# Kernel optimization log

Hardware: AMD Instinct MI355X
Metric: run time of the kernel (lower is better)

## Reference

```python
import jax, jax.numpy as jnp
import numpy as np

N = 20000        # nodes
E = 640000       # edges
D = 128          # embed_dim
L = 3            # num_layers
NUM_PROTEINS_MASK = 21
BN_EPS = 1e-5


def _batchnorm(x, gamma, beta):
    # training-mode BatchNorm1d: biased batch statistics over axis 0
    mu = jnp.mean(x, axis=0)
    var = jnp.mean((x - mu) ** 2, axis=0)
    return (x - mu) * jax.lax.rsqrt(var + BN_EPS) * gamma + beta


def setup_inputs() -> dict:
    key = jax.random.key(0)
    ks = jax.random.split(key, 20)
    s = 0.05
    return {
        "x_tokens": jax.random.randint(ks[0], (N,), 0, NUM_PROTEINS_MASK),
        "edge_index": jax.random.randint(ks[1], (2, E), 0, N),
        "edge_attr": jax.random.normal(ks[2], (E, D), jnp.float32),
        "emb": jax.random.normal(ks[3], (NUM_PROTEINS_MASK, D), jnp.float32) * s,
        "ee_W": jax.random.normal(ks[4], (L, D, D), jnp.float32) * s,
        "ee_b": jnp.zeros((L, D), jnp.float32),
        "W1": jax.random.normal(ks[5], (L, D, 2 * D), jnp.float32) * s,
        "b1": jnp.zeros((L, 2 * D), jnp.float32),
        "bn1_g": jnp.ones((L, 2 * D), jnp.float32),
        "bn1_b": jnp.zeros((L, 2 * D), jnp.float32),
        "W2": jax.random.normal(ks[6], (L, 2 * D, D), jnp.float32) * s,
        "b2": jnp.zeros((L, D), jnp.float32),
        "eps_p": jnp.zeros((L,), jnp.float32),
        "bn_g": jnp.ones((L, D), jnp.float32),
        "bn_b": jnp.zeros((L, D), jnp.float32),
    }


def reference(x_tokens, edge_index, edge_attr, emb, ee_W, ee_b, W1, b1,
              bn1_g, bn1_b, W2, b2, eps_p, bn_g, bn_b):
    src = edge_index[0]  # x_j is gathered from edge_index[0] (PyG source_to_target)
    dst = edge_index[1]
    h = emb[x_tokens]  # [N, D]
    for l in range(L):
        # GINConv: edge encode, gather-message-scatter
        ea = edge_attr @ ee_W[l] + ee_b[l]                      # [E, D]
        msg = jax.nn.relu(h[src] + ea)                          # [E, D]
        agg = jax.ops.segment_sum(msg, dst, num_segments=N)     # [N, D]
        z = (1.0 + eps_p[l]) * h + agg
        # MLP: Linear -> BN -> ReLU -> Linear
        z = _batchnorm(z @ W1[l] + b1[l], bn1_g[l], bn1_b[l])
        z = jax.nn.relu(z)
        h = z @ W2[l] + b2[l]
        # outer BatchNorm; ReLU except last layer; dropout p=0 -> identity
        h = _batchnorm(h, bn_g[l], bn_b[l])
        if l < L - 1:
            h = jax.nn.relu(h)
    return h
```

## Files before the change

### kernel.cpp

```cpp
#include <hip/hip_runtime.h>
#include <stdint.h>

#define NN 20000
#define EE 640000
#define DDIM 128
#define D2 256
#define NLAY 3
#define BN_EPS 1e-5f

typedef short bf16x8 __attribute__((ext_vector_type(8)));
typedef float f32x4 __attribute__((ext_vector_type(4)));

__device__ __forceinline__ short f2bf(float f) {
    uint32_t u = __float_as_uint(f);
    u += 0x7fff + ((u >> 16) & 1);
    return (short)(u >> 16);
}
__device__ __forceinline__ float bf2f(uint32_t u16) {
    return __uint_as_float(u16 << 16);
}

__global__ __launch_bounds__(256) void k_embed_hist(const int* __restrict__ tok,
                                                    const float* __restrict__ emb,
                                                    float* __restrict__ h,
                                                    const int* __restrict__ ei,
                                                    int* __restrict__ counts) {
    int gid = blockIdx.x * 256 + threadIdx.x;
    int r = gid >> 5;
    int c4 = gid & 31;
    int t = tok[r];
    ((float4*)h)[gid] = ((const float4*)emb)[t * 32 + c4];
    atomicAdd(&counts[ei[EE + gid]], 1);
}

__global__ __launch_bounds__(1024) void k_scan(const int* __restrict__ counts, int* __restrict__ cursor) {
    __shared__ int buf[NN];
    __shared__ int part[1024];
    int t = threadIdx.x;
    for (int i = t; i < NN; i += 1024) buf[i] = counts[i];
    __syncthreads();
    int base = t * 20;
    int s = 0;
    #pragma unroll
    for (int i = 0; i < 20; i++) {
        int idx = base + i;
        if (idx < NN) s += buf[idx];
    }
    part[t] = s;
    __syncthreads();
    for (int off = 1; off < 1024; off <<= 1) {
        int v = (t >= off) ? part[t - off] : 0;
        __syncthreads();
        part[t] += v;
        __syncthreads();
    }
    int run = part[t] - s;
    #pragma unroll
    for (int i = 0; i < 20; i++) {
        int idx = base + i;
        if (idx < NN) { int c = buf[idx]; buf[idx] = run; run += c; }
    }
    __syncthreads();
    for (int i = t; i < NN; i += 1024) cursor[i] = buf[i];
}

__global__ __launch_bounds__(256) void k_scatter(const int* __restrict__ ei,
                                                 int* __restrict__ cursor,
                                                 int* __restrict__ perm,
                                                 int* __restrict__ rank) {
    int e = blockIdx.x * 256 + threadIdx.x;
    int d = ei[EE + e];
    int pos = atomicAdd(&cursor[d], 1);
    perm[pos] = e;
    rank[e] = pos;
}

__global__ __launch_bounds__(256) void k_permute2(const float* __restrict__ edge_attr,
                                                  const int* __restrict__ ei,
                                                  const int* __restrict__ rank,
                                                  short* __restrict__ ea_bf,
                                                  int* __restrict__ srcs,
                                                  int* __restrict__ dsts) {
    int gid = blockIdx.x * 256 + threadIdx.x;
    int e = gid >> 5, c4 = gid & 31;
    float4 v = ((const float4*)edge_attr)[gid];
    int pos = rank[e];
    short4 b;
    b.x = f2bf(v.x); b.y = f2bf(v.y); b.z = f2bf(v.z); b.w = f2bf(v.w);
    ((short4*)ea_bf)[(size_t)pos * 32 + c4] = b;
    if (c4 == 0) { srcs[pos] = ei[e]; dsts[pos] = ei[EE + e]; }
}

__global__ __launch_bounds__(256) void k_prepw_all(const float* __restrict__ eeW,
                                                   const float* __restrict__ W1,
                                                   const float* __restrict__ W2,
                                                   short* __restrict__ WtE,
                                                   short* __restrict__ W1t,
                                                   short* __restrict__ W2t) {
    int gid = blockIdx.x * 256 + threadIdx.x;
    const int T1 = NLAY * 128 * 128;
    const int T2 = NLAY * 128 * 256;
    const int T3 = NLAY * 256 * 128;
    if (gid < T1) {
        int l = gid / (128 * 128), rem = gid % (128 * 128);
        int k = rem >> 7, n = rem & 127;
        WtE[(l * 128 + n) * 128 + k] = f2bf(eeW[gid]);
    } else if (gid < T1 + T2) {
        int g = gid - T1;
        int l = g / (128 * 256), rem = g % (128 * 256);
        int k = rem >> 8, n = rem & 255;
        W1t[(l * 256 + n) * 128 + k] = f2bf(W1[g]);
    } else if (gid < T1 + T2 + T3) {
        int g = gid - T1 - T2;
        int l = g / (256 * 128), rem = g % (256 * 128);
        int k = rem >> 7, n = rem & 127;
        W2t[(l * 128 + n) * 256 + k] = f2bf(W2[g]);
    }
}

__global__ __launch_bounds__(256) void k_edge3(const short* __restrict__ ea_bf,
                                               const int* __restrict__ srcs,
                                               const int* __restrict__ dsts,
                                               const short* __restrict__ WtL,
                                               const float* __restrict__ ebL,
                                               const float* __restrict__ hbase,
                                               const float* __restrict__ st2,
                                               const float* __restrict__ g2,
                                               const float* __restrict__ b2v,
                                               int lazy,
                                               float* __restrict__ agg) {
    __shared__ __align__(16) short sW[128 * 136];
    __shared__ __align__(16) short sOutB[64 * 132];
    __shared__ int sSrc[64], sDst[64];
    int tid = threadIdx.x;

    const uint2* wg = (const uint2*)WtL;
    #pragma unroll
    for (int i = 0; i < 16; i++) {
        int idx = tid + i * 256;
        uint2 v = wg[idx];
        int n = idx >> 5, k4 = (idx & 31) << 2;
        *(uint2*)&sW[n * 136 + k4] = v;
    }
    int lane = tid & 63, wv = tid >> 6;
    int l15 = lane & 15, quad = lane >> 4;
    int r0 = wv * 16;

    float ebv[8];
    #pragma unroll
    for (int nt = 0; nt < 8; nt++) ebv[nt] = ebL[nt * 16 + l15];

    int pc2 = tid & 63;
    int pc = pc2 * 2;
    int prb = tid >> 6;
    float ls0 = 0.f, ls1 = 0.f, lt0 = 0.f, lt1 = 0.f;
    if (lazy) {
        float inv_n = 1.f / (float)NN;
        float mu0 = st2[pc] * inv_n,     mu1 = st2[pc + 1] * inv_n;
        float va0 = st2[128 + pc] * inv_n - mu0 * mu0;
        float va1 = st2[129 + pc] * inv_n - mu1 * mu1;
        ls0 = g2[pc] * rsqrtf(va0 + BN_EPS);     lt0 = b2v[pc] - mu0 * ls0;
        ls1 = g2[pc + 1] * rsqrtf(va1 + BN_EPS); lt1 = b2v[pc + 1] - mu1 * ls1;
    }

    #pragma unroll 1
    for (int sub = 0; sub < 4; sub++) {
        int tile = blockIdx.x * 4 + sub;
        if (tid < 64) {
            sSrc[tid] = srcs[tile * 64 + tid];
            sDst[tid] = dsts[tile * 64 + tid];
        }
        const short* abase = ea_bf + ((size_t)(tile * 64 + r0 + l15)) * 128 + quad * 8;
        bf16x8 a[4];
        #pragma unroll
        for (int kt = 0; kt < 4; kt++) a[kt] = *(const bf16x8*)(abase + kt * 32);
        if (sub == 0) __syncthreads();

        f32x4 acc[8];
        #pragma unroll
        for (int i = 0; i < 8; i++) acc[i] = (f32x4){0.f, 0.f, 0.f, 0.f};
        #pragma unroll
        for (int kt = 0; kt < 4; kt++) {
            #pragma unroll
            for (int nt = 0; nt < 8; nt++) {
                bf16x8 b = *(const bf16x8*)&sW[(nt * 16 + l15) * 136 + kt * 32 + quad * 8];
                acc[nt] = __builtin_amdgcn_mfma_f32_16x16x32_bf16(a[kt], b, acc[nt], 0, 0, 0);
            }
        }
        #pragma unroll
        for (int nt = 0; nt < 8; nt++) {
            #pragma unroll
            for (int reg = 0; reg < 4; reg++)
                sOutB[(r0 + quad * 4 + reg) * 132 + nt * 16 + l15] = f2bf(acc[nt][reg] + ebv[nt]);
        }
        __syncthreads();

        #pragma unroll
        for (int i = 0; i < 16; i++) {
            int r = prb + i * 4;
            float2 hv = *(const float2*)&hbase[(size_t)sSrc[r] * DDIM + pc];
            float h0, h1;
            if (lazy) {
                h0 = fmaxf(hv.x * ls0 + lt0, 0.f);
                h1 = fmaxf(hv.y * ls1 + lt1, 0.f);
            } else {
                h0 = hv.x; h1 = hv.y;
            }
            uint32_t pp = *(uint32_t*)&sOutB[r * 132 + pc];
            float m0 = fmaxf(bf2f(pp & 0xffffu) + h0, 0.f);
            float m1 = fmaxf(bf2f(pp >> 16) + h1, 0.f);
            uint32_t po = (uint32_t)(uint16_t)f2bf(m0) | ((uint32_t)(uint16_t)f2bf(m1) << 16);
            *(uint32_t*)&sOutB[r * 132 + pc] = po;
        }
        __syncthreads();
        int c = tid & 127;
        int rbeg = (tid >> 7) * 32;
        float s = 0.f;
        int cur = sDst[rbeg];
        for (int r = rbeg; r < rbeg + 32; r++) {
            int d = sDst[r];
            if (d != cur) { atomicAdd(&agg[(size_t)cur * DDIM + c], s); s = 0.f; cur = d; }
            uint32_t raw = *(const uint16_t*)&sOutB[r * 132 + c];
            s += bf2f(raw);
        }
        atomicAdd(&agg[(size_t)cur * DDIM + c], s);
        if (sub < 3) __syncthreads();
    }
}

__global__ __launch_bounds__(256) void k_edge_g(const float* __restrict__ edge_attr,
                                                const short* __restrict__ WtL,
                                                const float* __restrict__ ebL,
                                                const float* __restrict__ h,
                                                const int* __restrict__ ei,
                                                const int* __restrict__ perm,
                                                float* __restrict__ agg) {
    __shared__ __align__(16) short sW[128 * 136];
    __shared__ __align__(16) char sU[64 * 132 * 4];
    __shared__ int sSrc[64], sDst[64], sEdge[64];
    short* sA = (short*)sU;
    float* sOut = (float*)sU;
    int tid = threadIdx.x;
    int tile = blockIdx.x;
    if (tid < 64) {
        int e = perm[tile * 64 + tid];
        sEdge[tid] = e;
        sSrc[tid] = ei[e];
        sDst[tid] = ei[EE + e];
    }
    const uint2* wg = (const uint2*)WtL;
    #pragma unroll
    for (int i = 0; i < 16; i++) {
        int idx = tid + i * 256;
        uint2 v = wg[idx];
        int n = idx >> 5, k4 = (idx & 31) << 2;
        *(uint2*)&sW[n * 136 + k4] = v;
    }
    __syncthreads();
    #pragma unroll
    for (int i = 0; i < 8; i++) {
        int idx = tid + i * 256;
        int r = idx >> 5, c4 = idx & 31;
        float4 v = ((const float4*)edge_attr)[sEdge[r] * 32 + c4];
        short4 b;
        b.x = f2bf(v.x); b.y = f2bf(v.y); b.z = f2bf(v.z); b.w = f2bf(v.w);
        *(short4*)&sA[r * 136 + (c4 << 2)] = b;
    }
    __syncthreads();
    int lane = tid & 63, wv = tid >> 6;
    int l15 = lane & 15, quad = lane >> 4;
    int r0 = wv * 16;
    f32x4 acc[8];
    #pragma unroll
    for (int i = 0; i < 8; i++) acc[i] = (f32x4){0.f, 0.f, 0.f, 0.f};
    #pragma unroll
    for (int kt = 0; kt < 4; kt++) {
        bf16x8 a = *(const bf16x8*)&sA[(r0 + l15) * 136 + kt * 32 + quad * 8];
        #pragma unroll
        for (int nt = 0; nt < 8; nt++) {
            bf16x8 b = *(const bf16x8*)&sW[(nt * 16 + l15) * 136 + kt * 32 + quad * 8];
            acc[nt] = __builtin_amdgcn_mfma_f32_16x16x32_bf16(a, b, acc[nt], 0, 0, 0);
        }
    }
    __syncthreads();
    #pragma unroll
    for (int nt = 0; nt < 8; nt++)
        #pragma unroll
        for (int reg = 0; reg < 4; reg++)
            sOut[(r0 + quad * 4 + reg) * 132 + nt * 16 + l15] = acc[nt][reg];
    __syncthreads();
    #pragma unroll
    for (int i = 0; i < 32; i++) {
        int idx = tid + i * 256;
        int r = idx >> 7, c = idx & 127;
        float v = sOut[r * 132 + c] + ebL[c] + h[(size_t)sSrc[r] * DDIM + c];
        sOut[r * 132 + c] = fmaxf(v, 0.f);
    }
    __syncthreads();
    int c = tid & 127;
    int rbeg = (tid >> 7) * 32;
    float s = 0.f;
    int cur = sDst[rbeg];
    for (int r = rbeg; r < rbeg + 32; r++) {
        int d = sDst[r];
        if (d != cur) { atomicAdd(&agg[(size_t)cur * DDIM + c], s); s = 0.f; cur = d; }
        s += sOut[r * 132 + c];
    }
    atomicAdd(&agg[(size_t)cur * DDIM + c], s);
}

__global__ __launch_bounds__(256) void k_gemm1z(const float* __restrict__ hbase,
                                                const float* __restrict__ st2,
                                                const float* __restrict__ g2,
                                                const float* __restrict__ b2v,
                                                int lazy,
                                                const float* __restrict__ agg,
                                                const float* __restrict__ epsP, int l,
                                                const short* __restrict__ W1tL,
                                                float* __restrict__ zz,
                                                float* __restrict__ stats) {
    __shared__ __align__(16) short sB[128 * 136];
    __shared__ __align__(16) short sA[64 * 136];
    int tid = threadIdx.x;
    int tile = blockIdx.x;
    int half = blockIdx.y;
    float e1 = 1.f + epsP[l];
    const uint2* bg = (const uint2*)W1tL + (size_t)half * 128 * 32;
    #pragma unroll
    for (int i = 0; i < 16; i++) {
        int idx = tid + i * 256;
        uint2 v = bg[idx];
        int n = idx >> 5, k4 = (idx & 31) << 2;
        *(uint2*)&sB[n * 136 + k4] = v;
    }
    {
        int c4 = tid & 31;
        int c = c4 * 4;
        float scv[4] = {0.f, 0.f, 0.f, 0.f}, shv[4] = {0.f, 0.f, 0.f, 0.f};
        if (lazy) {
            float inv_n = 1.f / (float)NN;
            #pragma unroll
            for (int j = 0; j < 4; j++) {
                float mu = st2[c + j] * inv_n;
                float var = st2[128 + c + j] * inv_n - mu * mu;
                float sc = g2[c + j] * rsqrtf(var + BN_EPS);
                scv[j] = sc;
                shv[j] = b2v[c + j] - mu * sc;
            }
        }
        #pragma unroll
        for (int i = 0; i < 8; i++) {
            int idx = tid + i * 256;
            int r = idx >> 5;
            int gr = tile * 64 + r;
            short4 o = {0, 0, 0, 0};
            if (gr < NN) {
                float4 hv = ((const float4*)hbase)[gr * 32 + c4];
                if (lazy) {
                    hv.x = fmaxf(hv.x * scv[0] + shv[0], 0.f);
                    hv.y = fmaxf(hv.y * scv[1] + shv[1], 0.f);
                    hv.z = fmaxf(hv.z * scv[2] + shv[2], 0.f);
                    hv.w = fmaxf(hv.w * scv[3] + shv[3], 0.f);
                }
                float4 av = ((const float4*)agg)[gr * 32 + c4];
                o.x = f2bf(e1 * hv.x + av.x);
                o.y = f2bf(e1 * hv.y + av.y);
                o.z = f2bf(e1 * hv.z + av.z);
                o.w = f2bf(e1 * hv.w + av.w);
            }
            *(short4*)&sA[r * 136 + c] = o;
        }
    }
    __syncthreads();
    int lane = tid & 63, wv = tid >> 6;
    int l15 = lane & 15, quad = lane >> 4;
    int r0 = wv * 16;
    f32x4 acc[8];
    #pragma unroll
    for (int i = 0; i < 8; i++) acc[i] = (f32x4){0.f, 0.f, 0.f, 0.f};
    #pragma unroll
    for (int kt = 0; kt < 4; kt++) {
        bf16x8 a = *(const bf16x8*)&sA[(r0 + l15) * 136 + kt * 32 + quad * 8];
        #pragma unroll
        for (int nt = 0; nt < 8; nt++) {
            bf16x8 b = *(const bf16x8*)&sB[(nt * 16 + l15) * 136 + kt * 32 + quad * 8];
            acc[nt] = __builtin_amdgcn_mfma_f32_16x16x32_bf16(a, b, acc[nt], 0, 0, 0);
        }
    }
    int grb = tile * 64 + r0 + quad * 4;
    #pragma unroll
    for (int nt = 0; nt < 8; nt++) {
        int col = half * 128 + nt * 16 + l15;
        float s = 0.f, s2 = 0.f;
        #pragma unroll
        for (int reg = 0; reg < 4; reg++) {
            int gr = grb + reg;
            float v = acc[nt][reg];
            s += v; s2 += v * v;
            if (gr < NN) zz[(size_t)gr * D2 + col] = v;
        }
        s += __shfl_xor(s, 16);  s += __shfl_xor(s, 32);
        s2 += __shfl_xor(s2, 16); s2 += __shfl_xor(s2, 32);
        if (quad == 0) {
            atomicAdd(&stats[col], s);
            atomicAdd(&stats[D2 + col], s2);
        }
    }
}

__global__ __launch_bounds__(256) void k_gemm2s(const float* __restrict__ zz,
                                                const short* __restrict__ W2tL,
                                                const float* __restrict__ st1,
                                                const float* __restrict__ g1,
                                                const float* __restrict__ b1v,
                                                float* __restrict__ h_pre,
                                                float* __restrict__ stats) {
    __shared__ __align__(16) short sB[64 * 136];
    __shared__ __align__(16) short sA[64 * 136];
    __shared__ float sSc[256], sSh[256];
    int tid = threadIdx.x;
    int tile = blockIdx.x;
    int half = blockIdx.y;
    int lane = tid & 63, wv = tid >> 6;
    int l15 = lane & 15, quad = lane >> 4;
    int r0 = wv * 16;
    f32x4 acc[4];
    #pragma unroll
    for (int i = 0; i < 4; i++) acc[i] = (f32x4){0.f, 0.f, 0.f, 0.f};

    #pragma unroll 1
    for (int p = 0; p < 2; p++) {
        if (p == 0) {
            float inv_n = 1.f / (float)NN;
            float mu = st1[tid] * inv_n;
            float var = st1[256 + tid] * inv_n - mu * mu;
            float sc = g1[tid] * rsqrtf(var + BN_EPS);
            sSc[tid] = sc;
            sSh[tid] = b1v[tid] - mu * sc;
            const uint2* bg = (const uint2*)W2tL + (size_t)half * 64 * 64;
            #pragma unroll
            for (int i = 0; i < 8; i++) {
                int idx = tid + i * 256;
                int n = idx >> 5, k4q = idx & 31;
                uint2 v = bg[n * 64 + k4q];
                *(uint2*)&sB[n * 136 + k4q * 4] = v;
            }
            __syncthreads();
        } else {
            __syncthreads();
            const uint2* bg = (const uint2*)W2tL + (size_t)half * 64 * 64 + 32;
            #pragma unroll
            for (int i = 0; i < 8; i++) {
                int idx = tid + i * 256;
                int n = idx >> 5, k4q = idx & 31;
                uint2 v = bg[n * 64 + k4q];
                *(uint2*)&sB[n * 136 + k4q * 4] = v;
            }
        }
        {
            int c4q = tid & 31;
            int cb = p * 128 + c4q * 4;
            #pragma unroll
            for (int i = 0; i < 8; i++) {
                int r = (tid >> 5) + i * 8;
                int gr = tile * 64 + r;
                short4 o = {0, 0, 0, 0};
                if (gr < NN) {
                    float4 v = ((const float4*)zz)[(size_t)gr * 64 + p * 32 + c4q];
                    o.x = f2bf(fmaxf(v.x * sSc[cb + 0] + sSh[cb + 0], 0.f));
                    o.y = f2bf(fmaxf(v.y * sSc[cb + 1] + sSh[cb + 1], 0.f));
                    o.z = f2bf(fmaxf(v.z * sSc[cb + 2] + sSh[cb + 2], 0.f));
                    o.w = f2bf(fmaxf(v.w * sSc[cb + 3] + sSh[cb + 3], 0.f));
                }
                *(short4*)&sA[r * 136 + c4q * 4] = o;
            }
        }
        __syncthreads();
        #pragma unroll
        for (int kt = 0; kt < 4; kt++) {
            bf16x8 a = *(const bf16x8*)&sA[(r0 + l15) * 136 + kt * 32 + quad * 8];
            #pragma unroll
            for (int nt = 0; nt < 4; nt++) {
                bf16x8 b = *(const bf16x8*)&sB[(nt * 16 + l15) * 136 + kt * 32 + quad * 8];
                acc[nt] = __builtin_amdgcn_mfma_f32_16x16x32_bf16(a, b, acc[nt], 0, 0, 0);
            }
        }
    }
    int grb = tile * 64 + r0 + quad * 4;
    #pragma unroll
    for (int nt = 0; nt < 4; nt++) {
        int col = half * 64 + nt * 16 + l15;
        float s = 0.f, s2 = 0.f;
        #pragma unroll
        for (int reg = 0; reg < 4; reg++) {
            int gr = grb + reg;
            float v = acc[nt][reg];
            s += v; s2 += v * v;
            if (gr < NN) h_pre[(size_t)gr * DDIM + col] = v;
        }
        s += __shfl_xor(s, 16);  s += __shfl_xor(s, 32);
        s2 += __shfl_xor(s2, 16); s2 += __shfl_xor(s2, 32);
        if (quad == 0) {
            atomicAdd(&stats[col], s);
            atomicAdd(&stats[DDIM + col], s2);
        }
    }
}

__global__ __launch_bounds__(256) void k_bn2(const float* __restrict__ h_pre,
                                             const float* __restrict__ st2,
                                             const float* __restrict__ g2,
                                             const float* __restrict__ b2v,
                                             int do_relu, float* __restrict__ dst) {
    int gid = blockIdx.x * 256 + threadIdx.x;
    int c0 = (gid & 31) << 2;
    float inv_n = 1.f / (float)NN;
    float4 v = ((const float4*)h_pre)[gid];
    float o[4];
    #pragma unroll
    for (int j = 0; j < 4; j++) {
        float mu = st2[c0 + j] * inv_n;
        float var = st2[128 + c0 + j] * inv_n - mu * mu;
        float sc = g2[c0 + j] * rsqrtf(var + BN_EPS);
        float sh = b2v[c0 + j] - mu * sc;
        float x = (&v.x)[j] * sc + sh;
        o[j] = do_relu ? fmaxf(x, 0.f) : x;
    }
    float4 ov = make_float4(o[0], o[1], o[2], o[3]);
    ((float4*)dst)[gid] = ov;
}

extern "C" void kernel_launch(void* const* d_in, const int* in_sizes, int n_in,
                              void* d_out, int out_size, void* d_ws, size_t ws_size,
                              hipStream_t stream) {
    const int*   tok       = (const int*)d_in[0];
    const int*   ei        = (const int*)d_in[1];
    const float* edge_attr = (const float*)d_in[2];
    const float* emb       = (const float*)d_in[3];
    const float* eeW       = (const float*)d_in[4];
    const float* eeB       = (const float*)d_in[5];
    const float* W1        = (const float*)d_in[6];
    const float* bn1g      = (const float*)d_in[8];
    const float* bn1b      = (const float*)d_in[9];
    const float* W2        = (const float*)d_in[10];
    const float* epsP      = (const float*)d_in[12];
    const float* bng       = (const float*)d_in[13];
    const float* bnb       = (const float*)d_in[14];
    float* out = (float*)d_out;

    char* ws = (char*)d_ws;
    size_t off = 0;
    auto alloc = [&](size_t bytes) -> char* {
        off = (off + 511) & ~(size_t)511;
        char* p = ws + off;
        off += bytes;
        return p;
    };
    float* h      = (float*)alloc((size_t)NN * DDIM * 4);
    float* aggs   = (float*)alloc(((size_t)NN * DDIM + 512) * 4);
    float* agg    = aggs;
    float* stats1 = aggs + (size_t)NN * DDIM;
    float* zz     = (float*)alloc((size_t)NN * D2 * 4);
    float* h_pre  = (float*)alloc((size_t)NN * DDIM * 4);
    int*   perm   = (int*)alloc((size_t)EE * 4);
    int*   rank   = (int*)alloc((size_t)EE * 4);
    int*   counts = (int*)alloc((size_t)NN * 4);
    int*   cursor = (int*)alloc((size_t)NN * 4);
    int*   srcs   = (int*)alloc((size_t)EE * 4);
    int*   dsts   = (int*)alloc((size_t)EE * 4);
    short* WtE    = (short*)alloc((size_t)NLAY * 128 * 128 * 2);
    short* W1t    = (short*)alloc((size_t)NLAY * 128 * 256 * 2);
    short* W2t    = (short*)alloc((size_t)NLAY * 256 * 128 * 2);
    float* stats2 = (float*)alloc(512 * 4);
    short* ea_bf  = (short*)alloc((size_t)EE * DDIM * 2);
    bool big = (off <= ws_size);
    (void)in_sizes; (void)n_in; (void)out_size;

    hipMemsetAsync(counts, 0, (size_t)NN * 4, stream);
    k_prepw_all<<<960, 256, 0, stream>>>(eeW, W1, W2, WtE, W1t, W2t);
    k_embed_hist<<<2500, 256, 0, stream>>>(tok, emb, h, ei, counts);
    k_scan<<<1, 1024, 0, stream>>>(counts, cursor);
    k_scatter<<<2500, 256, 0, stream>>>(ei, cursor, perm, rank);
    if (big) {
        k_permute2<<<EE * 32 / 256, 256, 0, stream>>>(edge_attr, ei, rank, ea_bf, srcs, dsts);
    }

    for (int l = 0; l < NLAY; l++) {
        hipMemsetAsync(aggs, 0, ((size_t)NN * DDIM + 512) * 4, stream);
        float* st2cur  = stats2 + (l & 1) * 256;
        float* st2prev = stats2 + ((l + 1) & 1) * 256;
        hipMemsetAsync(st2cur, 0, 256 * 4, stream);
        int lazy = (big && l > 0) ? 1 : 0;
        const float* hb  = lazy ? h_pre : h;
        int lp = (l > 0) ? (l - 1) : 0;
        const float* g2p = bng + (size_t)lp * 128;
        const float* b2p = bnb + (size_t)lp * 128;
        if (big) {
            k_edge3<<<EE / 256, 256, 0, stream>>>(ea_bf, srcs, dsts,
                                                  WtE + (size_t)l * 128 * 128,
                                                  eeB + (size_t)l * 128,
                                                  hb, st2prev, g2p, b2p, lazy, agg);
        } else {
            k_edge_g<<<EE / 64, 256, 0, stream>>>(edge_attr, WtE + (size_t)l * 128 * 128,
                                                  eeB + (size_t)l * 128, h, ei, perm, agg);
        }
        k_gemm1z<<<dim3((NN + 63) / 64, 2), 256, 0, stream>>>(hb, st2prev, g2p, b2p, lazy, agg,
                                                              epsP, l,
                                                              W1t + (size_t)l * 128 * 256, zz, stats1);
        k_gemm2s<<<dim3((NN + 63) / 64, 2), 256, 0, stream>>>(zz, W2t + (size_t)l * 256 * 128,
                                                              stats1, bn1g + (size_t)l * 256,
                                                              bn1b + (size_t)l * 256, h_pre, st2cur);
        if (big) {
            if (l == NLAY - 1)
                k_bn2<<<2500, 256, 0, stream>>>(h_pre, st2cur, bng + (size_t)l * 128,
                                                bnb + (size_t)l * 128, 0, out);
        } else {
            k_bn2<<<2500, 256, 0, stream>>>(h_pre, st2cur, bng + (size_t)l * 128,
                                            bnb + (size_t)l * 128, (l < NLAY - 1) ? 1 : 0,
                                            (l == NLAY - 1) ? out : h);
        }
    }
}
```

Measured before the change: 1.179 ms.

## Materialize bf16 normalized node features and prefetch next edge tile in edge kernel

Replaces the lazy BatchNorm-on-gather scheme with an explicit k_bn2 pass that writes post-BN/ReLU node features as bf16. Edge and GEMM1 kernels then gather half-size bf16 rows with no per-element affine work. The edge kernel also processes 8 tiles per block and double-buffers src/dst indices while prefetching the next tile's A fragments into registers during the current tile's MFMA. The costs are an extra bn2 launch per layer, more register pressure from the prefetch buffers, and bf16 rounding of h before aggregation.

```diff
diff --git a/kernel.cpp b/kernel.cpp
--- a/kernel.cpp
+++ b/kernel.cpp
@@ -7,6 +7,7 @@
 #define D2 256
 #define NLAY 3
 #define BN_EPS 1e-5f
+#define SUBS 8
 
 typedef short bf16x8 __attribute__((ext_vector_type(8)));
 typedef float f32x4 __attribute__((ext_vector_type(4)));
@@ -22,14 +23,17 @@
 
 __global__ __launch_bounds__(256) void k_embed_hist(const int* __restrict__ tok,
                                                     const float* __restrict__ emb,
-                                                    float* __restrict__ h,
+                                                    short* __restrict__ h_bn,
                                                     const int* __restrict__ ei,
                                                     int* __restrict__ counts) {
     int gid = blockIdx.x * 256 + threadIdx.x;
     int r = gid >> 5;
     int c4 = gid & 31;
     int t = tok[r];
-    ((float4*)h)[gid] = ((const float4*)emb)[t * 32 + c4];
+    float4 e = ((const float4*)emb)[t * 32 + c4];
+    short4 o;
+    o.x = f2bf(e.x); o.y = f2bf(e.y); o.z = f2bf(e.z); o.w = f2bf(e.w);
+    ((short4*)h_bn)[gid] = o;
     atomicAdd(&counts[ei[EE + gid]], 1);
 }
 
@@ -123,16 +127,13 @@
                                                const int* __restrict__ dsts,
                                                const short* __restrict__ WtL,
                                                const float* __restrict__ ebL,
-                                               const float* __restrict__ hbase,
-                                               const float* __restrict__ st2,
-                                               const float* __restrict__ g2,
-                                               const float* __restrict__ b2v,
-                                               int lazy,
+                                               const short* __restrict__ h_bn,
                                                float* __restrict__ agg) {
     __shared__ __align__(16) short sW[128 * 136];
     __shared__ __align__(16) short sOutB[64 * 132];
-    __shared__ int sSrc[64], sDst[64];
+    __shared__ int sSrc[2][64], sDst[2][64];
     int tid = threadIdx.x;
+    int tile0 = blockIdx.x * SUBS;
 
     const uint2* wg = (const uint2*)WtL;
     #pragma unroll
@@ -145,37 +146,25 @@
     int lane = tid & 63, wv = tid >> 6;
     int l15 = lane & 15, quad = lane >> 4;
     int r0 = wv * 16;
-
     float ebv[8];
     #pragma unroll
     for (int nt = 0; nt < 8; nt++) ebv[nt] = ebL[nt * 16 + l15];
-
-    int pc2 = tid & 63;
-    int pc = pc2 * 2;
+    int pc = (tid & 63) * 2;
     int prb = tid >> 6;
-    float ls0 = 0.f, ls1 = 0.f, lt0 = 0.f, lt1 = 0.f;
-    if (lazy) {
-        float inv_n = 1.f / (float)NN;
-        float mu0 = st2[pc] * inv_n,     mu1 = st2[pc + 1] * inv_n;
-        float va0 = st2[128 + pc] * inv_n - mu0 * mu0;
-        float va1 = st2[129 + pc] * inv_n - mu1 * mu1;
-        ls0 = g2[pc] * rsqrtf(va0 + BN_EPS);     lt0 = b2v[pc] - mu0 * ls0;
-        ls1 = g2[pc + 1] * rsqrtf(va1 + BN_EPS); lt1 = b2v[pc + 1] - mu1 * ls1;
-    }
+
+    if (tid < 64) {
+        sSrc[0][tid] = srcs[tile0 * 64 + tid];
+        sDst[0][tid] = dsts[tile0 * 64 + tid];
+    }
+    const short* abase = ea_bf + ((size_t)tile0 * 64 + r0 + l15) * 128 + quad * 8;
+    bf16x8 a[4];
+    #pragma unroll
+    for (int kt = 0; kt < 4; kt++) a[kt] = *(const bf16x8*)(abase + kt * 32);
+    __syncthreads();
 
     #pragma unroll 1
-    for (int sub = 0; sub < 4; sub++) {
-        int tile = blockIdx.x * 4 + sub;
-        if (tid < 64) {
-            sSrc[tid] = srcs[tile * 64 + tid];
-            sDst[tid] = dsts[tile * 64 + tid];
-        }
-        const short* abase = ea_bf + ((size_t)(tile * 64 + r0 + l15)) * 128 + quad * 8;
-        bf16x8 a[4];
-        #pragma unroll
-        for (int kt = 0; kt < 4; kt++) a[kt] = *(const bf16x8*)(abase + kt * 32);
-        if (sub == 0) __syncthreads();
-
+    for (int sub = 0; sub < SUBS; sub++) {
+        int buf = sub & 1;
         f32x4 acc[8];
         #pragma unroll
         for (int i = 0; i < 8; i++) acc[i] = (f32x4){0.f, 0.f, 0.f, 0.f};
@@ -187,6 +176,16 @@
                 acc[nt] = __builtin_amdgcn_mfma_f32_16x16x32_bf16(a[kt], b, acc[nt], 0, 0, 0);
             }
         }
+        bf16x8 an[4];
+        if (sub + 1 < SUBS) {
+            const short* nb = abase + (size_t)(sub + 1) * 64 * 128;
+            #pragma unroll
+            for (int kt = 0; kt < 4; kt++) an[kt] = *(const bf16x8*)(nb + kt * 32);
+            if (tid < 64) {
+                sSrc[buf ^ 1][tid] = srcs[(tile0 + sub + 1) * 64 + tid];
+                sDst[buf ^ 1][tid] = dsts[(tile0 + sub + 1) * 64 + tid];
+            }
+        }
         #pragma unroll
         for (int nt = 0; nt < 8; nt++) {
             #pragma unroll
@@ -198,17 +197,10 @@
         #pragma unroll
         for (int i = 0; i < 16; i++) {
             int r = prb + i * 4;
-            float2 hv = *(const float2*)&hbase[(size_t)sSrc[r] * DDIM + pc];
-            float h0, h1;
-            if (lazy) {
-                h0 = fmaxf(hv.x * ls0 + lt0, 0.f);
-                h1 = fmaxf(hv.y * ls1 + lt1, 0.f);
-            } else {
-                h0 = hv.x; h1 = hv.y;
-            }
+            uint32_t hb = *(const uint32_t*)&h_bn[(size_t)sSrc[buf][r] * DDIM + pc];
             uint32_t pp = *(uint32_t*)&sOutB[r * 132 + pc];
-            float m0 = fmaxf(bf2f(pp & 0xffffu) + h0, 0.f);
-            float m1 = fmaxf(bf2f(pp >> 16) + h1, 0.f);
+            float m0 = fmaxf(bf2f(pp & 0xffffu) + bf2f(hb & 0xffffu), 0.f);
+            float m1 = fmaxf(bf2f(pp >> 16) + bf2f(hb >> 16), 0.f);
             uint32_t po = (uint32_t)(uint16_t)f2bf(m0) | ((uint32_t)(uint16_t)f2bf(m1) << 16);
             *(uint32_t*)&sOutB[r * 132 + pc] = po;
         }
@@ -216,22 +208,25 @@
         int c = tid & 127;
         int rbeg = (tid >> 7) * 32;
         float s = 0.f;
-        int cur = sDst[rbeg];
+        int cur = sDst[buf][rbeg];
         for (int r = rbeg; r < rbeg + 32; r++) {
-            int d = sDst[r];
+            int d = sDst[buf][r];
             if (d != cur) { atomicAdd(&agg[(size_t)cur * DDIM + c], s); s = 0.f; cur = d; }
-            uint32_t raw = *(const uint16_t*)&sOutB[r * 132 + c];
-            s += bf2f(raw);
+            s += bf2f(*(const uint16_t*)&sOutB[r * 132 + c]);
         }
         atomicAdd(&agg[(size_t)cur * DDIM + c], s);
-        if (sub < 3) __syncthreads();
+        if (sub + 1 < SUBS) {
+            #pragma unroll
+            for (int kt = 0; kt < 4; kt++) a[kt] = an[kt];
+            __syncthreads();
+        }
     }
 }
 
 __global__ __launch_bounds__(256) void k_edge_g(const float* __restrict__ edge_attr,
                                                 const short* __restrict__ WtL,
                                                 const float* __restrict__ ebL,
-                                                const float* __restrict__ h,
+                                                const short* __restrict__ h_bn,
                                                 const int* __restrict__ ei,
                                                 const int* __restrict__ perm,
                                                 float* __restrict__ agg) {
@@ -293,7 +288,8 @@
     for (int i = 0; i < 32; i++) {
         int idx = tid + i * 256;
         int r = idx >> 7, c = idx & 127;
-        float v = sOut[r * 132 + c] + ebL[c] + h[(size_t)sSrc[r] * DDIM + c];
+        float hv = bf2f(*(const uint16_t*)&h_bn[(size_t)sSrc[r] * DDIM + c]);
+        float v = sOut[r * 132 + c] + ebL[c] + hv;
         sOut[r * 132 + c] = fmaxf(v, 0.f);
     }
     __syncthreads();
@@ -309,11 +305,7 @@
     atomicAdd(&agg[(size_t)cur * DDIM + c], s);
 }
 
-__global__ __launch_bounds__(256) void k_gemm1z(const float* __restrict__ hbase,
-                                                const float* __restrict__ st2,
-                                                const float* __restrict__ g2,
-                                                const float* __restrict__ b2v,
-                                                int lazy,
+__global__ __launch_bounds__(256) void k_gemm1z(const short* __restrict__ h_bn,
                                                 const float* __restrict__ agg,
                                                 const float* __restrict__ epsP, int l,
                                                 const short* __restrict__ W1tL,
@@ -336,18 +328,6 @@
     {
         int c4 = tid & 31;
         int c = c4 * 4;
-        float scv[4] = {0.f, 0.f, 0.f, 0.f}, shv[4] = {0.f, 0.f, 0.f, 0.f};
-        if (lazy) {
-            float inv_n = 1.f / (float)NN;
-            #pragma unroll
-            for (int j = 0; j < 4; j++) {
-                float mu = st2[c + j] * inv_n;
-                float var = st2[128 + c + j] * inv_n - mu * mu;
-                float sc = g2[c + j] * rsqrtf(var + BN_EPS);
-                scv[j] = sc;
-                shv[j] = b2v[c + j] - mu * sc;
-            }
-        }
         #pragma unroll
         for (int i = 0; i < 8; i++) {
             int idx = tid + i * 256;
@@ -355,18 +335,12 @@
             int gr = tile * 64 + r;
             short4 o = {0, 0, 0, 0};
             if (gr < NN) {
-                float4 hv = ((const float4*)hbase)[gr * 32 + c4];
-                if (lazy) {
-                    hv.x = fmaxf(hv.x * scv[0] + shv[0], 0.f);
-                    hv.y = fmaxf(hv.y * scv[1] + shv[1], 0.f);
-                    hv.z = fmaxf(hv.z * scv[2] + shv[2], 0.f);
-                    hv.w = fmaxf(hv.w * scv[3] + shv[3], 0.f);
-                }
-                float4 av = ((const float4*)agg)[gr * 32 + c4];
-                o.x = f2bf(e1 * hv.x + av.x);
-                o.y = f2bf(e1 * hv.y + av.y);
-                o.z = f2bf(e1 * hv.z + av.z);
-                o.w = f2bf(e1 * hv.w + av.w);
+                ushort4 hb = ((const ushort4*)h_bn)[(size_t)gr * 32 + c4];
+                float4 av = ((const float4*)agg)[(size_t)gr * 32 + c4];
+                o.x = f2bf(e1 * bf2f(hb.x) + av.x);
+                o.y = f2bf(e1 * bf2f(hb.y) + av.y);
+                o.z = f2bf(e1 * bf2f(hb.z) + av.z);
+                o.w = f2bf(e1 * bf2f(hb.w) + av.w);
             }
             *(short4*)&sA[r * 136 + c] = o;
         }
@@ -511,7 +485,8 @@
                                              const float* __restrict__ st2,
                                              const float* __restrict__ g2,
                                              const float* __restrict__ b2v,
-                                             int do_relu, float* __restrict__ dst) {
+                                             int do_relu, float* __restrict__ dst,
+                                             short* __restrict__ dst16, int write16) {
     int gid = blockIdx.x * 256 + threadIdx.x;
     int c0 = (gid & 31) << 2;
     float inv_n = 1.f / (float)NN;
@@ -526,8 +501,13 @@
         float x = (&v.x)[j] * sc + sh;
         o[j] = do_relu ? fmaxf(x, 0.f) : x;
     }
-    float4 ov = make_float4(o[0], o[1], o[2], o[3]);
-    ((float4*)dst)[gid] = ov;
+    if (write16) {
+        short4 ob;
+        ob.x = f2bf(o[0]); ob.y = f2bf(o[1]); ob.z = f2bf(o[2]); ob.w = f2bf(o[3]);
+        ((short4*)dst16)[gid] = ob;
+    } else {
+        ((float4*)dst)[gid] = make_float4(o[0], o[1], o[2], o[3]);
+    }
 }
 
 extern "C" void kernel_launch(void* const* d_in, const int* in_sizes, int n_in,
@@ -556,10 +536,11 @@
         off += bytes;
         return p;
     };
-    float* h      = (float*)alloc((size_t)NN * DDIM * 4);
-    float* aggs   = (float*)alloc(((size_t)NN * DDIM + 512) * 4);
+    short* h_bn   = (short*)alloc((size_t)NN * DDIM * 2);
+    float* aggs   = (float*)alloc(((size_t)NN * DDIM + 768) * 4);
     float* agg    = aggs;
     float* stats1 = aggs + (size_t)NN * DDIM;
+    float* stats2 = stats1 + 512;
     float* zz     = (float*)alloc((size_t)NN * D2 * 4);
     float* h_pre  = (float*)alloc((size_t)NN * DDIM * 4);
     int*   perm   = (int*)alloc((size_t)EE * 4);
@@ -571,14 +552,13 @@
     short* WtE    = (short*)alloc((size_t)NLAY * 128 * 128 * 2);
     short* W1t    = (short*)alloc((size_t)NLAY * 128 * 256 * 2);
     short* W2t    = (short*)alloc((size_t)NLAY * 256 * 128 * 2);
-    float* stats2 = (float*)alloc(512 * 4);
     short* ea_bf  = (short*)alloc((size_t)EE * DDIM * 2);
     bool big = (off <= ws_size);
     (void)in_sizes; (void)n_in; (void)out_size;
 
     hipMemsetAsync(counts, 0, (size_t)NN * 4, stream);
     k_prepw_all<<<960, 256, 0, stream>>>(eeW, W1, W2, WtE, W1t, W2t);
-    k_embed_hist<<<2500, 256, 0, stream>>>(tok, emb, h, ei, counts);
+    k_embed_hist<<<2500, 256, 0, stream>>>(tok, emb, h_bn, ei, counts);
     k_scan<<<1, 1024, 0, stream>>>(counts, cursor);
     k_scatter<<<2500, 256, 0, stream>>>(ei, cursor, perm, rank);
     if (big) {
@@ -586,38 +566,24 @@
     }
 
     for (int l = 0; l < NLAY; l++) {
-        hipMemsetAsync(aggs, 0, ((size_t)NN * DDIM + 512) * 4, stream);
-        float* st2cur  = stats2 + (l & 1) * 256;
-        float* st2prev = stats2 + ((l + 1) & 1) * 256;
-        hipMemsetAsync(st2cur, 0, 256 * 4, stream);
-        int lazy = (big && l > 0) ? 1 : 0;
-        const float* hb  = lazy ? h_pre : h;
-        int lp = (l > 0) ? (l - 1) : 0;
-        const float* g2p = bng + (size_t)lp * 128;
-        const float* b2p = bnb + (size_t)lp * 128;
+        hipMemsetAsync(aggs, 0, ((size_t)NN * DDIM + 768) * 4, stream);
         if (big) {
-            k_edge3<<<EE / 256, 256, 0, stream>>>(ea_bf, srcs, dsts,
-                                                  WtE + (size_t)l * 128 * 128,
-                                                  eeB + (size_t)l * 128,
-                                                  hb, st2prev, g2p, b2p, lazy, agg);
+            k_edge3<<<EE / (64 * SUBS), 256, 0, stream>>>(ea_bf, srcs, dsts,
+                                                          WtE + (size_t)l * 128 * 128,
+                                                          eeB + (size_t)l * 128, h_bn, agg);
         } else {
             k_edge_g<<<EE / 64, 256, 0, stream>>>(edge_attr, WtE + (size_t)l * 128 * 128,
-                                                  eeB + (size_t)l * 128, h, ei, perm, agg);
-        }
-        k_gemm1z<<<dim3((NN + 63) / 64, 2), 256, 0, stream>>>(hb, st2prev, g2p, b2p, lazy, agg,
-                                                              epsP, l,
+                                                  eeB + (size_t)l * 128, h_bn, ei, perm, agg);
+        }
+        k_gemm1z<<<dim3((NN + 63) / 64, 2), 256, 0, stream>>>(h_bn, agg, epsP, l,
                                                               W1t + (size_t)l * 128 * 256, zz, stats1);
         k_gemm2s<<<dim3((NN + 63) / 64, 2), 256, 0, stream>>>(zz, W2t + (size_t)l * 256 * 128,
                                                               stats1, bn1g + (size_t)l * 256,
-                                                              bn1b + (size_t)l * 256, h_pre, st2cur);
-        if (big) {
-            if (l == NLAY - 1)
-                k_bn2<<<2500, 256, 0, stream>>>(h_pre, st2cur, bng + (size_t)l * 128,
-                                                bnb + (size_t)l * 128, 0, out);
-        } else {
-            k_bn2<<<2500, 256, 0, stream>>>(h_pre, st2cur, bng + (size_t)l * 128,
-                                            bnb + (size_t)l * 128, (l < NLAY - 1) ? 1 : 0,
-                                            (l == NLAY - 1) ? out : h);
-        }
-    }
-}
+                                                              bn1b + (size_t)l * 256, h_pre, stats2);
+        int last = (l == NLAY - 1);
+        k_bn2<<<2500, 256, 0, stream>>>(h_pre, stats2, bng + (size_t)l * 128,
+                                        bnb + (size_t)l * 128,
+                                        last ? 0 : 1, last ? out : nullptr,
+                                        h_bn, last ? 0 : 1);
+    }
+}
```

New measurement: 1.173 ms. No clear change (-0.5%).
